# Optimization experiments

Hardware: AMD Instinct MI355X
Metric: run time of the kernel (lower is better)

Reference implementation:

```python
import jax, jax.numpy as jnp
import numpy as np

NUM_HEADS = 64
D_K = 8  # n_wires of the quantum circuit


def setup_inputs() -> dict:
    key = jax.random.key(0)
    k1, k2, k3 = jax.random.split(key, 3)
    B, S, E = 8, 8192, NUM_HEADS * D_K
    x = jax.random.normal(k1, (B, S, E), dtype=jnp.float32)
    # trainable RX rotation angles, one per wire, shared across heads
    theta = jax.random.normal(k2, (D_K,), dtype=jnp.float32)
    # out_proj weight (torch nn.Linear stores [out_features, in_features]); bias=False
    W_out = jax.random.normal(k3, (E, E), dtype=jnp.float32) * 0.02
    return {"x": x, "theta": theta, "W_out": W_out}


def reference(x, theta, W_out):
    B, S, E = x.shape
    H, d = NUM_HEADS, D_K
    # Quantum circuit per (batch, seq, head) element:
    # RX(x_i) then RX(theta_i) on wire i from |0>, <Z_i> = cos(x_i + theta_i).
    xr = x.reshape(B, S, H, d)               # (B, S, H, d_k)
    A = jnp.cos(xr + theta)                  # broadcast theta over wires
    # torch stacks heads first -> (B, H, S, d), then .view(B, S, E) on the
    # contiguous buffer (a memory-layout reinterpretation, not a head-merge).
    A = jnp.transpose(A, (0, 2, 1, 3)).reshape(B, S, E)
    # out_proj: y = A @ W^T (no bias)
    return A @ W_out.T
```

## Files before the change

kernel.cpp:

```cpp
#include <hip/hip_runtime.h>
#include <hip/hip_bf16.h>

typedef __attribute__((ext_vector_type(8))) short short8;
typedef __attribute__((ext_vector_type(4))) float float4v;
typedef __attribute__((ext_vector_type(4))) unsigned int uint4v;
typedef __attribute__((ext_vector_type(2))) unsigned int uint2v;

#define SS 8192
#define EE 512
#define HH 64
#define NKB 16

__device__ __forceinline__ unsigned int f2bf1(float f) {
    unsigned int u = __builtin_bit_cast(unsigned int, f);
    return (u + 0x7fffu + ((u >> 16) & 1u)) >> 16;
}
__device__ __forceinline__ unsigned int pack2(float lo, float hi) {
    return f2bf1(lo) | (f2bf1(hi) << 16);
}
__device__ __forceinline__ void gl_lds16(const void* g, void* l) {
    __builtin_amdgcn_global_load_lds(
        (const __attribute__((address_space(1))) void*)g,
        (__attribute__((address_space(3))) void*)l, 16, 0, 0);
}

__global__ void w_prep(const float* __restrict__ W, unsigned short* __restrict__ Wws) {
    int idx = blockIdx.x * 256 + threadIdx.x;
    int r  = idx >> 7;
    int kg = idx & 127;
    int k  = kg * 4;
    float4v v = *(const float4v*)(W + (size_t)r * EE + k);
    int ntile = r >> 7, n = r & 127, kb = k >> 5, kk = k & 31;
    unsigned short* dst = Wws + (((size_t)(ntile * 16 + kb) * 128 + n) * 32 + kk);
    uint2v pk = { pack2(v.x, v.y), pack2(v.z, v.w) };
    *(uint2v*)dst = pk;
}

__global__ __launch_bounds__(256, 2)
void qmha_fused3(const float* __restrict__ x, const float* __restrict__ theta,
                 const unsigned short* __restrict__ Wws, float* __restrict__ out)
{
    __shared__ __attribute__((aligned(16))) unsigned short A_lds[HH * 512];
    __shared__ __attribute__((aligned(16))) unsigned short W_lds[2][128 * 32];

    const int bx    = blockIdx.x;
    const int ntile = (bx >> 3) & 3;
    const int p     = ((bx >> 5) << 3) | (bx & 7);
    const int b     = p >> 7;
    const int sc    = p & 127;

    const int t = threadIdx.x, lane = t & 63, wid = t >> 6;

    const unsigned short* Wtile = Wws + (size_t)ntile * 16 * 4096;
    const int woff = wid * 1024 + lane * 8;
    const unsigned short* wsrc = Wtile + woff;

    short8 wa[4], wb[4];
    #pragma unroll
    for (int s = 0; s < 4; ++s) {
        wa[s] = *(const short8*)(wsrc + (size_t)s * 4096);
        wb[s] = *(const short8*)(wsrc + (size_t)s * 4096 + 512);
    }

    const float th0 = theta[0], th1 = theta[1], th2 = theta[2], th3 = theta[3];
    const float th4 = theta[4], th5 = theta[5], th6 = theta[6], th7 = theta[7];

    {
        const float* xb = x + ((size_t)b * SS + (size_t)sc * 64) * EE + lane * 8;
        const int sw = lane & 7;
        #pragma unroll
        for (int it = 0; it < 16; ++it) {
            const int s_loc = wid * 16 + it;
            const float* px = xb + (size_t)s_loc * EE;
            float4v v0 = *(const float4v*)(px);
            float4v v1 = *(const float4v*)(px + 4);
            float c0 = __cosf(v0.x + th0);
            float c1 = __cosf(v0.y + th1);
            float c2 = __cosf(v0.z + th2);
            float c3 = __cosf(v0.w + th3);
            float c4 = __cosf(v1.x + th4);
            float c5 = __cosf(v1.y + th5);
            float c6 = __cosf(v1.z + th6);
            float c7 = __cosf(v1.w + th7);
            uint4v pk = { pack2(c0,c1), pack2(c2,c3), pack2(c4,c5), pack2(c6,c7) };
            *(uint4v*)&A_lds[lane * 512 + ((s_loc ^ sw) * 8)] = pk;
        }
    }

    float4v acc[2][4];
    #pragma unroll
    for (int i = 0; i < 2; ++i)
        #pragma unroll
        for (int j = 0; j < 4; ++j)
            acc[i][j] = (float4v){0.f, 0.f, 0.f, 0.f};

    const int m0  = (wid >> 1) * 32;
    const int n0l = (wid & 1) * 64;
    const int fr  = lane & 15;
    const int q   = lane >> 4;
    const int swA = fr & 7;
    const int aBase0 = (m0 + fr) * 512;
    const int aBase1 = aBase0 + 16 * 512;
    const int bOff   = (n0l + fr) * 32 + q * 8;

    asm volatile("s_waitcnt lgkmcnt(0)" ::: "memory");
    __builtin_amdgcn_s_barrier();

    #pragma unroll
    for (int kb = 0; kb < NKB; ++kb) {
        unsigned short* Wd = (unsigned short*)W_lds[kb & 1] + woff;
        *(short8*)(Wd)       = wa[kb & 3];
        *(short8*)(Wd + 512) = wb[kb & 3];
        if (kb + 4 < NKB) {
            wa[kb & 3] = *(const short8*)(wsrc + (size_t)(kb + 4) * 4096);
            wb[kb & 3] = *(const short8*)(wsrc + (size_t)(kb + 4) * 4096 + 512);
        }
        asm volatile("s_waitcnt lgkmcnt(0)" ::: "memory");
        __builtin_amdgcn_s_barrier();
        asm volatile("" ::: "memory");

        const unsigned short* Bbuf = (const unsigned short*)W_lds[kb & 1];
        const int g = ((kb * 4 + q) ^ swA) * 8;

        short8 a0 = *(const short8*)&A_lds[aBase0 + g];
        short8 a1 = *(const short8*)&A_lds[aBase1 + g];
        short8 b0 = *(const short8*)&Bbuf[bOff + 0 * 16 * 32];
        short8 b1 = *(const short8*)&Bbuf[bOff + 1 * 16 * 32];
        short8 b2 = *(const short8*)&Bbuf[bOff + 2 * 16 * 32];
        short8 b3 = *(const short8*)&Bbuf[bOff + 3 * 16 * 32];

        __builtin_amdgcn_s_setprio(1);
        acc[0][0] = __builtin_amdgcn_mfma_f32_16x16x32_bf16(a0, b0, acc[0][0], 0, 0, 0);
        acc[0][1] = __builtin_amdgcn_mfma_f32_16x16x32_bf16(a0, b1, acc[0][1], 0, 0, 0);
        acc[0][2] = __builtin_amdgcn_mfma_f32_16x16x32_bf16(a0, b2, acc[0][2], 0, 0, 0);
        acc[0][3] = __builtin_amdgcn_mfma_f32_16x16x32_bf16(a0, b3, acc[0][3], 0, 0, 0);
        acc[1][0] = __builtin_amdgcn_mfma_f32_16x16x32_bf16(a1, b0, acc[1][0], 0, 0, 0);
        acc[1][1] = __builtin_amdgcn_mfma_f32_16x16x32_bf16(a1, b1, acc[1][1], 0, 0, 0);
        acc[1][2] = __builtin_amdgcn_mfma_f32_16x16x32_bf16(a1, b2, acc[1][2], 0, 0, 0);
        acc[1][3] = __builtin_amdgcn_mfma_f32_16x16x32_bf16(a1, b3, acc[1][3], 0, 0, 0);
        __builtin_amdgcn_s_setprio(0);
    }

    const int colbase = ntile * 128 + n0l + fr;
    #pragma unroll
    for (int mt = 0; mt < 2; ++mt) {
        #pragma unroll
        for (int r = 0; r < 4; ++r) {
            const int hrow = m0 + mt * 16 + q * 4 + r;
            float* po = out + ((size_t)b * SS + (size_t)hrow * 128 + sc) * EE + colbase;
            po[0 * 16] = acc[mt][0][r];
            po[1 * 16] = acc[mt][1][r];
            po[2 * 16] = acc[mt][2][r];
            po[3 * 16] = acc[mt][3][r];
        }
    }
}

#define AS 520
#define WSF 40
__global__ __launch_bounds__(256, 2)
void qmha_fused_fb(const float* __restrict__ x, const float* __restrict__ theta,
                   const float* __restrict__ W, float* __restrict__ out)
{
    __shared__ __attribute__((aligned(16))) unsigned short A_lds[HH * AS];
    __shared__ __attribute__((aligned(16))) unsigned short W_lds[128 * WSF];
    const int bx = blockIdx.x;
    const int ntile = (bx >> 3) & 3;
    const int p = ((bx >> 5) << 3) | (bx & 7);
    const int b = p >> 7;
    const int sc = p & 127;
    const int t = threadIdx.x, lane = t & 63, wid = t >> 6;
    const int wn = t >> 1, wk = (t & 1) * 16;
    const float* Wbase = W + (size_t)(ntile * 128 + wn) * EE + wk;
    float4v wv0 = *(const float4v*)(Wbase + 0);
    float4v wv1 = *(const float4v*)(Wbase + 4);
    float4v wv2 = *(const float4v*)(Wbase + 8);
    float4v wv3 = *(const float4v*)(Wbase + 12);
    const float th0 = theta[0], th1 = theta[1], th2 = theta[2], th3 = theta[3];
    const float th4 = theta[4], th5 = theta[5], th6 = theta[6], th7 = theta[7];
    {
        const float* xb = x + ((size_t)b * SS + (size_t)sc * 64) * EE + lane * 8;
        #pragma unroll
        for (int it = 0; it < 16; ++it) {
            const int s_loc = wid * 16 + it;
            const float* px = xb + (size_t)s_loc * EE;
            float4v v0 = *(const float4v*)(px);
            float4v v1 = *(const float4v*)(px + 4);
            float c0 = __cosf(v0.x + th0), c1 = __cosf(v0.y + th1);
            float c2 = __cosf(v0.z + th2), c3 = __cosf(v0.w + th3);
            float c4 = __cosf(v1.x + th4), c5 = __cosf(v1.y + th5);
            float c6 = __cosf(v1.z + th6), c7 = __cosf(v1.w + th7);
            uint4v pk = { pack2(c0,c1), pack2(c2,c3), pack2(c4,c5), pack2(c6,c7) };
            *(uint4v*)&A_lds[lane * AS + s_loc * 8] = pk;
        }
    }
    float4v acc[2][4];
    #pragma unroll
    for (int i = 0; i < 2; ++i)
        #pragma unroll
        for (int j = 0; j < 4; ++j)
            acc[i][j] = (float4v){0.f, 0.f, 0.f, 0.f};
    const int m0 = (wid >> 1) * 32, n0l = (wid & 1) * 64;
    const int fr = lane & 15, q = lane >> 4;
    const unsigned short* Arow0 = &A_lds[(m0 + fr) * AS + q * 8];
    const unsigned short* Arow1 = Arow0 + 16 * AS;
    const unsigned short* Wrow  = &W_lds[(n0l + fr) * WSF + q * 8];
    for (int kb = 0; kb < NKB; ++kb) {
        __syncthreads();
        {
            uint4v lo = { pack2(wv0.x, wv0.y), pack2(wv0.z, wv0.w),
                          pack2(wv1.x, wv1.y), pack2(wv1.z, wv1.w) };
            uint4v hi = { pack2(wv2.x, wv2.y), pack2(wv2.z, wv2.w),
                          pack2(wv3.x, wv3.y), pack2(wv3.z, wv3.w) };
            *(uint4v*)&W_lds[wn * WSF + wk]     = lo;
            *(uint4v*)&W_lds[wn * WSF + wk + 8] = hi;
        }
        if (kb < NKB - 1) {
            const float* Wn = Wbase + (size_t)(kb + 1) * 32;
            wv0 = *(const float4v*)(Wn + 0);
            wv1 = *(const float4v*)(Wn + 4);
            wv2 = *(const float4v*)(Wn + 8);
            wv3 = *(const float4v*)(Wn + 12);
        }
        __syncthreads();
        short8 a0 = *(const short8*)(Arow0 + kb * 32);
        short8 a1 = *(const short8*)(Arow1 + kb * 32);
        short8 b0 = *(const short8*)(Wrow + 0 * 16 * WSF);
        short8 b1 = *(const short8*)(Wrow + 1 * 16 * WSF);
        short8 b2 = *(const short8*)(Wrow + 2 * 16 * WSF);
        short8 b3 = *(const short8*)(Wrow + 3 * 16 * WSF);
        acc[0][0] = __builtin_amdgcn_mfma_f32_16x16x32_bf16(a0, b0, acc[0][0], 0, 0, 0);
        acc[0][1] = __builtin_amdgcn_mfma_f32_16x16x32_bf16(a0, b1, acc[0][1], 0, 0, 0);
        acc[0][2] = __builtin_amdgcn_mfma_f32_16x16x32_bf16(a0, b2, acc[0][2], 0, 0, 0);
        acc[0][3] = __builtin_amdgcn_mfma_f32_16x16x32_bf16(a0, b3, acc[0][3], 0, 0, 0);
        acc[1][0] = __builtin_amdgcn_mfma_f32_16x16x32_bf16(a1, b0, acc[1][0], 0, 0, 0);
        acc[1][1] = __builtin_amdgcn_mfma_f32_16x16x32_bf16(a1, b1, acc[1][1], 0, 0, 0);
        acc[1][2] = __builtin_amdgcn_mfma_f32_16x16x32_bf16(a1, b2, acc[1][2], 0, 0, 0);
        acc[1][3] = __builtin_amdgcn_mfma_f32_16x16x32_bf16(a1, b3, acc[1][3], 0, 0, 0);
    }
    const int colbase = ntile * 128 + n0l + fr;
    #pragma unroll
    for (int mt = 0; mt < 2; ++mt) {
        #pragma unroll
        for (int r = 0; r < 4; ++r) {
            const int hrow = m0 + mt * 16 + q * 4 + r;
            float* po = out + ((size_t)b * SS + (size_t)hrow * 128 + sc) * EE + colbase;
            po[0 * 16] = acc[mt][0][r];
            po[1 * 16] = acc[mt][1][r];
            po[2 * 16] = acc[mt][2][r];
            po[3 * 16] = acc[mt][3][r];
        }
    }
}

extern "C" void kernel_launch(void* const* d_in, const int* in_sizes, int n_in,
                              void* d_out, int out_size, void* d_ws, size_t ws_size,
                              hipStream_t stream) {
    const float* x     = (const float*)d_in[0];
    const float* theta = (const float*)d_in[1];
    const float* W     = (const float*)d_in[2];
    float* out         = (float*)d_out;

    if (ws_size >= (size_t)EE * EE * sizeof(unsigned short)) {
        unsigned short* Wws = (unsigned short*)d_ws;
        w_prep<<<dim3(256), dim3(256), 0, stream>>>(W, Wws);
        qmha_fused3<<<dim3(4096), dim3(256), 0, stream>>>(x, theta, Wws, out);
    } else {
        qmha_fused_fb<<<dim3(4096), dim3(256), 0, stream>>>(x, theta, W, out);
    }
}
```

Measured before the change: 274.3 us.

## Compute full N per block with async W streaming and pipelined cosine A tiles

Each block now computes all 512 output columns for its 64 rows instead of a 128-column slice, so x is read and the cosine is evaluated once per element rather than four times across n-tiles. W tiles are streamed directly into LDS with global_load_lds into a double buffer, using an XOR swizzle set up by the prep kernel, and the cosine of the next k-slice is computed while the current MFMAs run. The grid shrinks to 1024 blocks and each thread holds many more accumulators, which raises register pressure and may lower occupancy.

```diff
diff --git a/kernel.cpp b/kernel.cpp
--- a/kernel.cpp
+++ b/kernel.cpp
@@ -8,8 +8,8 @@
 
 #define SS 8192
 #define EE 512
-#define HH 64
 #define NKB 16
+#define APAD 40
 
 __device__ __forceinline__ unsigned int f2bf1(float f) {
     unsigned int u = __builtin_bit_cast(unsigned int, f);
@@ -24,140 +24,181 @@
         (__attribute__((address_space(3))) void*)l, 16, 0, 0);
 }
 
+#define WAITV(n) asm volatile("s_waitcnt vmcnt(" #n ")" ::: "memory")
+#define WAITL()  asm volatile("s_waitcnt lgkmcnt(0)" ::: "memory")
+#define MEMBAR() asm volatile("" ::: "memory")
+
 __global__ void w_prep(const float* __restrict__ W, unsigned short* __restrict__ Wws) {
     int idx = blockIdx.x * 256 + threadIdx.x;
-    int r  = idx >> 7;
+    int n  = idx >> 7;
     int kg = idx & 127;
     int k  = kg * 4;
-    float4v v = *(const float4v*)(W + (size_t)r * EE + k);
-    int ntile = r >> 7, n = r & 127, kb = k >> 5, kk = k & 31;
-    unsigned short* dst = Wws + (((size_t)(ntile * 16 + kb) * 128 + n) * 32 + kk);
+    float4v v = *(const float4v*)(W + (size_t)n * EE + k);
+    int kb = k >> 5, kl = k & 31;
+    int slot = ((kl >> 3) ^ ((n >> 1) & 3));
+    int j = kl & 7;
+    unsigned short* dst = Wws + ((size_t)kb * (EE * 32) + (size_t)n * 32 + slot * 8 + j);
     uint2v pk = { pack2(v.x, v.y), pack2(v.z, v.w) };
     *(uint2v*)dst = pk;
 }
 
 __global__ __launch_bounds__(256, 2)
-void qmha_fused3(const float* __restrict__ x, const float* __restrict__ theta,
+void qmha_fused4(const float* __restrict__ x, const float* __restrict__ theta,
                  const unsigned short* __restrict__ Wws, float* __restrict__ out)
 {
-    __shared__ __attribute__((aligned(16))) unsigned short A_lds[HH * 512];
-    __shared__ __attribute__((aligned(16))) unsigned short W_lds[2][128 * 32];
-
-    const int bx    = blockIdx.x;
-    const int ntile = (bx >> 3) & 3;
-    const int p     = ((bx >> 5) << 3) | (bx & 7);
-    const int b     = p >> 7;
-    const int sc    = p & 127;
-
+    __shared__ __attribute__((aligned(16))) unsigned short W_lds[2][EE * 32];
+    __shared__ __attribute__((aligned(16))) unsigned short A_lds[2][64 * APAD];
+
+    const int bx = blockIdx.x;
+    const int b  = bx >> 7;
+    const int sc = bx & 127;
     const int t = threadIdx.x, lane = t & 63, wid = t >> 6;
-
-    const unsigned short* Wtile = Wws + (size_t)ntile * 16 * 4096;
-    const int woff = wid * 1024 + lane * 8;
-    const unsigned short* wsrc = Wtile + woff;
-
-    short8 wa[4], wb[4];
-    #pragma unroll
-    for (int s = 0; s < 4; ++s) {
-        wa[s] = *(const short8*)(wsrc + (size_t)s * 4096);
-        wb[s] = *(const short8*)(wsrc + (size_t)s * 4096 + 512);
-    }
+    const int fr = lane & 15, q = lane >> 4;
+
+    const unsigned short* wsrc_base = Wws + (size_t)wid * 4096 + lane * 8;
+    const int wdst_off = wid * 4096 + lane * 8;
+
+    const float* xrow_base = x + ((size_t)b * SS + (size_t)sc * 64 + wid) * EE + lane * 8;
+
+    const int aw_off = lane * APAD + wid * 8;
+
+    const int aoff = fr * APAD + q * 8;
+    const int boff = (wid * 128 + fr) * 32 + ((q ^ ((fr >> 1) & 3)) * 8);
 
     const float th0 = theta[0], th1 = theta[1], th2 = theta[2], th3 = theta[3];
     const float th4 = theta[4], th5 = theta[5], th6 = theta[6], th7 = theta[7];
 
+    float4v acc[4][8];
+    #pragma unroll
+    for (int i = 0; i < 4; ++i)
+        #pragma unroll
+        for (int j2 = 0; j2 < 8; ++j2)
+            acc[i][j2] = (float4v){0.f, 0.f, 0.f, 0.f};
+
+#define ISSUE_W(kbv) do { \
+    const unsigned short* _s = wsrc_base + (size_t)(kbv) * (EE * 32); \
+    unsigned short* _d = (unsigned short*)W_lds[(kbv) & 1] + wdst_off; \
+    gl_lds16(_s + 0 * 512, _d + 0 * 512); \
+    gl_lds16(_s + 1 * 512, _d + 1 * 512); \
+    gl_lds16(_s + 2 * 512, _d + 2 * 512); \
+    gl_lds16(_s + 3 * 512, _d + 3 * 512); \
+    gl_lds16(_s + 4 * 512, _d + 4 * 512); \
+    gl_lds16(_s + 5 * 512, _d + 5 * 512); \
+    gl_lds16(_s + 6 * 512, _d + 6 * 512); \
+    gl_lds16(_s + 7 * 512, _d + 7 * 512); \
+} while (0)
+
+#define COS_WRITE(kbv, va, vb) do { \
+    float _c0 = __cosf((va).x + th0), _c1 = __cosf((va).y + th1); \
+    float _c2 = __cosf((va).z + th2), _c3 = __cosf((va).w + th3); \
+    float _c4 = __cosf((vb).x + th4), _c5 = __cosf((vb).y + th5); \
+    float _c6 = __cosf((vb).z + th6), _c7 = __cosf((vb).w + th7); \
+    uint4v _pk = { pack2(_c0,_c1), pack2(_c2,_c3), pack2(_c4,_c5), pack2(_c6,_c7) }; \
+    *(uint4v*)&A_lds[(kbv) & 1][aw_off] = _pk; \
+} while (0)
+
+    float4v xA0, xA1, xB0, xB1;
+    { const float* _p = xrow_base;              xA0 = *(const float4v*)_p; xA1 = *(const float4v*)(_p + 4); }
+    MEMBAR();
+    ISSUE_W(0);
+    MEMBAR();
+    { const float* _p = xrow_base + 4 * EE;     xB0 = *(const float4v*)_p; xB1 = *(const float4v*)(_p + 4); }
+    MEMBAR();
+    ISSUE_W(1);
+    MEMBAR();
+    WAITV(18);
+    COS_WRITE(0, xA0, xA1);
+    WAITV(10);
+    WAITL();
+    __builtin_amdgcn_s_barrier();
+
+#define BODY_FULL(kbv, xCa, xCb, xNa, xNb) do { \
+    { const float* _p = xrow_base + (size_t)((kbv) + 2) * (4 * EE); \
+      xNa = *(const float4v*)_p; xNb = *(const float4v*)(_p + 4); }             \
+    MEMBAR(); \
+    const unsigned short* _Ab = A_lds[(kbv) & 1]; \
+    const unsigned short* _Bb = W_lds[(kbv) & 1]; \
+    short8 _af[4], _bf[8]; \
+    _Pragma("unroll") for (int _mt = 0; _mt < 4; ++_mt) \
+        _af[_mt] = *(const short8*)&_Ab[aoff + _mt * 16 * APAD]; \
+    _Pragma("unroll") for (int _nt = 0; _nt < 8; ++_nt) \
+        _bf[_nt] = *(const short8*)&_Bb[boff + _nt * 512]; \
+    WAITL();                     \
+    ISSUE_W((kbv) + 2);                                                          \
+    MEMBAR(); \
+    __builtin_amdgcn_s_setprio(1); \
+    _Pragma("unroll") for (int _nt = 0; _nt < 8; ++_nt) \
+        _Pragma("unroll") for (int _mt = 0; _mt < 4; ++_mt) \
+            acc[_mt][_nt] = __builtin_amdgcn_mfma_f32_16x16x32_bf16(_af[_mt], _bf[_nt], acc[_mt][_nt], 0, 0, 0); \
+    __builtin_amdgcn_s_setprio(0); \
+    WAITV(18);                   \
+    COS_WRITE((kbv) + 1, xCa, xCb); \
+    WAITV(10);                   \
+    WAITL(); \
+    __builtin_amdgcn_s_barrier(); \
+} while (0)
+
+    for (int kb = 0; kb < 14; kb += 2) {
+        BODY_FULL(kb,     xB0, xB1, xA0, xA1);
+        BODY_FULL(kb + 1, xA0, xA1, xB0, xB1);
+    }
+
     {
-        const float* xb = x + ((size_t)b * SS + (size_t)sc * 64) * EE + lane * 8;
-        const int sw = lane & 7;
-        #pragma unroll
-        for (int it = 0; it < 16; ++it) {
-            const int s_loc = wid * 16 + it;
-            const float* px = xb + (size_t)s_loc * EE;
-            float4v v0 = *(const float4v*)(px);
-            float4v v1 = *(const float4v*)(px + 4);
-            float c0 = __cosf(v0.x + th0);
-            float c1 = __cosf(v0.y + th1);
-            float c2 = __cosf(v0.z + th2);
-            float c3 = __cosf(v0.w + th3);
-            float c4 = __cosf(v1.x + th4);
-            float c5 = __cosf(v1.y + th5);
-            float c6 = __cosf(v1.z + th6);
-            float c7 = __cosf(v1.w + th7);
-            uint4v pk = { pack2(c0,c1), pack2(c2,c3), pack2(c4,c5), pack2(c6,c7) };
-            *(uint4v*)&A_lds[lane * 512 + ((s_loc ^ sw) * 8)] = pk;
-        }
-    }
-
-    float4v acc[2][4];
+        const unsigned short* _Ab = A_lds[0];
+        const unsigned short* _Bb = W_lds[0];
+        short8 _af[4], _bf[8];
+        #pragma unroll
+        for (int _mt = 0; _mt < 4; ++_mt) _af[_mt] = *(const short8*)&_Ab[aoff + _mt * 16 * APAD];
+        #pragma unroll
+        for (int _nt = 0; _nt < 8; ++_nt) _bf[_nt] = *(const short8*)&_Bb[boff + _nt * 512];
+        __builtin_amdgcn_s_setprio(1);
+        #pragma unroll
+        for (int _nt = 0; _nt < 8; ++_nt)
+            #pragma unroll
+            for (int _mt = 0; _mt < 4; ++_mt)
+                acc[_mt][_nt] = __builtin_amdgcn_mfma_f32_16x16x32_bf16(_af[_mt], _bf[_nt], acc[_mt][_nt], 0, 0, 0);
+        __builtin_amdgcn_s_setprio(0);
+        WAITV(8);
+        COS_WRITE(15, xB0, xB1);
+        WAITV(0);
+        WAITL();
+        __builtin_amdgcn_s_barrier();
+    }
+    {
+        const unsigned short* _Ab = A_lds[1];
+        const unsigned short* _Bb = W_lds[1];
+        short8 _af[4], _bf[8];
+        #pragma unroll
+        for (int _mt = 0; _mt < 4; ++_mt) _af[_mt] = *(const short8*)&_Ab[aoff + _mt * 16 * APAD];
+        #pragma unroll
+        for (int _nt = 0; _nt < 8; ++_nt) _bf[_nt] = *(const short8*)&_Bb[boff + _nt * 512];
+        #pragma unroll
+        for (int _nt = 0; _nt < 8; ++_nt)
+            #pragma unroll
+            for (int _mt = 0; _mt < 4; ++_mt)
+                acc[_mt][_nt] = __builtin_amdgcn_mfma_f32_16x16x32_bf16(_af[_mt], _bf[_nt], acc[_mt][_nt], 0, 0, 0);
+    }
+
+    float* outb = out + (size_t)b * (SS * EE) + (size_t)sc * EE + wid * 128 + fr;
     #pragma unroll
-    for (int i = 0; i < 2; ++i)
-        #pragma unroll
-        for (int j = 0; j < 4; ++j)
-            acc[i][j] = (float4v){0.f, 0.f, 0.f, 0.f};
-
-    const int m0  = (wid >> 1) * 32;
-    const int n0l = (wid & 1) * 64;
-    const int fr  = lane & 15;
-    const int q   = lane >> 4;
-    const int swA = fr & 7;
-    const int aBase0 = (m0 + fr) * 512;
-    const int aBase1 = aBase0 + 16 * 512;
-    const int bOff   = (n0l + fr) * 32 + q * 8;
-
-    asm volatile("s_waitcnt lgkmcnt(0)" ::: "memory");
-    __builtin_amdgcn_s_barrier();
-
-    #pragma unroll
-    for (int kb = 0; kb < NKB; ++kb) {
-        unsigned short* Wd = (unsigned short*)W_lds[kb & 1] + woff;
-        *(short8*)(Wd)       = wa[kb & 3];
-        *(short8*)(Wd + 512) = wb[kb & 3];
-        if (kb + 4 < NKB) {
-            wa[kb & 3] = *(const short8*)(wsrc + (size_t)(kb + 4) * 4096);
-            wb[kb & 3] = *(const short8*)(wsrc + (size_t)(kb + 4) * 4096 + 512);
-        }
-        asm volatile("s_waitcnt lgkmcnt(0)" ::: "memory");
-        __builtin_amdgcn_s_barrier();
-        asm volatile("" ::: "memory");
-
-        const unsigned short* Bbuf = (const unsigned short*)W_lds[kb & 1];
-        const int g = ((kb * 4 + q) ^ swA) * 8;
-
-        short8 a0 = *(const short8*)&A_lds[aBase0 + g];
-        short8 a1 = *(const short8*)&A_lds[aBase1 + g];
-        short8 b0 = *(const short8*)&Bbuf[bOff + 0 * 16 * 32];
-        short8 b1 = *(const short8*)&Bbuf[bOff + 1 * 16 * 32];
-        short8 b2 = *(const short8*)&Bbuf[bOff + 2 * 16 * 32];
-        short8 b3 = *(const short8*)&Bbuf[bOff + 3 * 16 * 32];
-
-        __builtin_amdgcn_s_setprio(1);
-        acc[0][0] = __builtin_amdgcn_mfma_f32_16x16x32_bf16(a0, b0, acc[0][0], 0, 0, 0);
-        acc[0][1] = __builtin_amdgcn_mfma_f32_16x16x32_bf16(a0, b1, acc[0][1], 0, 0, 0);
-        acc[0][2] = __builtin_amdgcn_mfma_f32_16x16x32_bf16(a0, b2, acc[0][2], 0, 0, 0);
-        acc[0][3] = __builtin_amdgcn_mfma_f32_16x16x32_bf16(a0, b3, acc[0][3], 0, 0, 0);
-        acc[1][0] = __builtin_amdgcn_mfma_f32_16x16x32_bf16(a1, b0, acc[1][0], 0, 0, 0);
-        acc[1][1] = __builtin_amdgcn_mfma_f32_16x16x32_bf16(a1, b1, acc[1][1], 0, 0, 0);
-        acc[1][2] = __builtin_amdgcn_mfma_f32_16x16x32_bf16(a1, b2, acc[1][2], 0, 0, 0);
-        acc[1][3] = __builtin_amdgcn_mfma_f32_16x16x32_bf16(a1, b3, acc[1][3], 0, 0, 0);
-        __builtin_amdgcn_s_setprio(0);
-    }
-
-    const int colbase = ntile * 128 + n0l + fr;
-    #pragma unroll
-    for (int mt = 0; mt < 2; ++mt) {
+    for (int mt = 0; mt < 4; ++mt) {
         #pragma unroll
         for (int r = 0; r < 4; ++r) {
-            const int hrow = m0 + mt * 16 + q * 4 + r;
-            float* po = out + ((size_t)b * SS + (size_t)hrow * 128 + sc) * EE + colbase;
-            po[0 * 16] = acc[mt][0][r];
-            po[1 * 16] = acc[mt][1][r];
-            po[2 * 16] = acc[mt][2][r];
-            po[3 * 16] = acc[mt][3][r];
-        }
-    }
+            const int m = mt * 16 + q * 4 + r;
+            float* po = outb + (size_t)m * (128 * EE);
+            #pragma unroll
+            for (int nt = 0; nt < 8; ++nt)
+                po[nt * 16] = acc[mt][nt][r];
+        }
+    }
+#undef BODY_FULL
+#undef ISSUE_W
+#undef COS_WRITE
 }
 
 #define AS 520
 #define WSF 40
+#define HH 64
 __global__ __launch_bounds__(256, 2)
 void qmha_fused_fb(const float* __restrict__ x, const float* __restrict__ theta,
                    const float* __restrict__ W, float* __restrict__ out)
@@ -264,7 +305,7 @@
     if (ws_size >= (size_t)EE * EE * sizeof(unsigned short)) {
         unsigned short* Wws = (unsigned short*)d_ws;
         w_prep<<<dim3(256), dim3(256), 0, stream>>>(W, Wws);
-        qmha_fused3<<<dim3(4096), dim3(256), 0, stream>>>(x, theta, Wws, out);
+        qmha_fused4<<<dim3(1024), dim3(256), 0, stream>>>(x, theta, Wws, out);
     } else {
         qmha_fused_fb<<<dim3(4096), dim3(256), 0, stream>>>(x, theta, W, out);
     }
```

Result: faster. 246.7 us (-10.1%).
